# Performance work log

Hardware: AMD Instinct MI355X
Metric: run time of the kernel (lower is better)

Reference implementation:

```python
import jax, jax.numpy as jnp
import numpy as np

N_NODES = 100000
N_EDGES = 1250000
D_IN, D_HID, D_OUT = 64, 32, 41


def setup_inputs() -> dict:
    key = jax.random.key(0)
    ks = jax.random.split(key, 7)
    x = jax.random.normal(ks[0], (N_NODES, D_IN), dtype=jnp.float32)
    edge_index = jax.random.randint(ks[1], (2, N_EDGES), 0, N_NODES, dtype=jnp.int64)
    # PyG SAGEConv params: lin_l (applied to aggregated neighbors, has bias),
    # lin_r (applied to root, no bias). Stored here as [in, out] matrices.
    W1l = jax.random.normal(ks[2], (D_IN, D_HID), dtype=jnp.float32) / np.sqrt(D_IN)
    b1 = jnp.zeros((D_HID,), dtype=jnp.float32)
    W1r = jax.random.normal(ks[3], (D_IN, D_HID), dtype=jnp.float32) / np.sqrt(D_IN)
    W2l = jax.random.normal(ks[4], (D_HID, D_OUT), dtype=jnp.float32) / np.sqrt(D_HID)
    b2 = jnp.zeros((D_OUT,), dtype=jnp.float32)
    W2r = jax.random.normal(ks[5], (D_HID, D_OUT), dtype=jnp.float32) / np.sqrt(D_HID)
    return {"x": x, "edge_index": edge_index, "W1l": W1l, "b1": b1, "W1r": W1r,
            "W2l": W2l, "b2": b2, "W2r": W2r}


def _sage_conv(h, src, dst, n_nodes, Wl, b, Wr):
    # mean-aggregate source features at destination nodes (PyG default aggr='mean')
    msg = h[src]  # [E, d] irregular gather
    agg = jax.ops.segment_sum(msg, dst, num_segments=n_nodes)
    cnt = jax.ops.segment_sum(jnp.ones((src.shape[0],), dtype=h.dtype), dst,
                              num_segments=n_nodes)
    agg = agg / jnp.maximum(cnt, 1.0)[:, None]
    return agg @ Wl + b + h @ Wr


def reference(x, edge_index, W1l, b1, W1r, W2l, b2, W2r):
    src, dst = edge_index[0], edge_index[1]
    n = x.shape[0]
    h = _sage_conv(x, src, dst, n, W1l, b1, W1r)
    h = jax.nn.relu(h)
    # F.dropout(training=self.training) -> identity in eval/inference mode
    out = _sage_conv(h, src, dst, n, W2l, b2, W2r)
    return out
```

## Files before the change

### kernel.cpp

```cpp
#include <hip/hip_runtime.h>

#define N_NODES 100000
#define N_EDGES 1250000
#define D_IN 64
#define D_HID 32
#define D_OUT 41
#define NBUK 784
#define BSH 7
#define BCAP 1920
#define BBLK 192
#define BCHUNK 6511
#define PBLK 1563
#define ROWCAP 48
#define LCAP 52
#define LSTR 88
#define ZERO_OFF 6400000

typedef short bf16x8 __attribute__((ext_vector_type(8)));
typedef float f32x4 __attribute__((ext_vector_type(4)));

__device__ __forceinline__ float bflo(unsigned int u) {
    union { unsigned int i; float f; } v; v.i = u << 16; return v.f;
}
__device__ __forceinline__ float bfhi(unsigned int u) {
    union { unsigned int i; float f; } v; v.i = u & 0xffff0000u; return v.f;
}
__device__ __forceinline__ unsigned short f2bf(float f) {
    union { float f; unsigned int i; } v; v.f = f;
    unsigned int x = v.i;
    return (unsigned short)((x + 0x7fffu + ((x >> 16) & 1u)) >> 16);
}
__device__ __forceinline__ void acc8(float* a, uint4 u) {
    a[0] += bflo(u.x); a[1] += bfhi(u.x);
    a[2] += bflo(u.y); a[3] += bfhi(u.y);
    a[4] += bflo(u.z); a[5] += bfhi(u.z);
    a[6] += bflo(u.w); a[7] += bfhi(u.w);
}

__device__ __forceinline__ void lds_sort(const unsigned int* bk, int total,
                                         int* lists, int* lcnt, int tid) {
    if (tid < 128) lcnt[tid] = 0;
    __syncthreads();
    int i = tid;
    for (; i + 768 < total; i += 1024) {
        unsigned int w0 = bk[i];
        unsigned int w1 = bk[i + 256];
        unsigned int w2 = bk[i + 512];
        unsigned int w3 = bk[i + 768];
        int d0 = (int)(w0 >> 17), s0 = atomicAdd(&lcnt[d0], 1);
        if (s0 < ROWCAP) lists[d0 * LCAP + s0] = (int)((w0 & 0x1FFFFu) << 6);
        int d1 = (int)(w1 >> 17), s1 = atomicAdd(&lcnt[d1], 1);
        if (s1 < ROWCAP) lists[d1 * LCAP + s1] = (int)((w1 & 0x1FFFFu) << 6);
        int d2 = (int)(w2 >> 17), s2 = atomicAdd(&lcnt[d2], 1);
        if (s2 < ROWCAP) lists[d2 * LCAP + s2] = (int)((w2 & 0x1FFFFu) << 6);
        int d3 = (int)(w3 >> 17), s3 = atomicAdd(&lcnt[d3], 1);
        if (s3 < ROWCAP) lists[d3 * LCAP + s3] = (int)((w3 & 0x1FFFFu) << 6);
    }
    for (; i < total; i += 256) {
        unsigned int w = bk[i];
        int dl = (int)(w >> 17);
        int slot = atomicAdd(&lcnt[dl], 1);
        if (slot < ROWCAP) lists[dl * LCAP + slot] = (int)((w & 0x1FFFFu) << 6);
    }
    __syncthreads();
    if (tid < 128) {
        int c = lcnt[tid];
        int cc = c < ROWCAP ? c : ROWCAP;
        int ce = (cc + 15) & ~15; if (ce > ROWCAP) ce = ROWCAP;
        for (int s = cc; s < ce; ++s) lists[tid * LCAP + s] = ZERO_OFF;
    }
    __syncthreads();
}

__device__ __forceinline__ void gather_node(const int* row, int d, const char* tab,
                                            int qb, float* a) {
    int dd = d < ROWCAP ? d : ROWCAP;
    int ddp = (dd + 15) & ~15; if (ddp > ROWCAP) ddp = ROWCAP;
    for (int i = 0; i < ddp; i += 16) {
        int4 o0 = *(const int4*)(row + i);
        int4 o1 = *(const int4*)(row + i + 4);
        int4 o2 = *(const int4*)(row + i + 8);
        int4 o3 = *(const int4*)(row + i + 12);
        uint4 u0 = *(const uint4*)(tab + o0.x + qb);
        uint4 u1 = *(const uint4*)(tab + o0.y + qb);
        uint4 u2 = *(const uint4*)(tab + o0.z + qb);
        uint4 u3 = *(const uint4*)(tab + o0.w + qb);
        uint4 u4 = *(const uint4*)(tab + o1.x + qb);
        uint4 u5 = *(const uint4*)(tab + o1.y + qb);
        uint4 u6 = *(const uint4*)(tab + o1.z + qb);
        uint4 u7 = *(const uint4*)(tab + o1.w + qb);
        uint4 u8 = *(const uint4*)(tab + o2.x + qb);
        uint4 u9 = *(const uint4*)(tab + o2.y + qb);
        uint4 ua = *(const uint4*)(tab + o2.z + qb);
        uint4 ub = *(const uint4*)(tab + o2.w + qb);
        uint4 uc = *(const uint4*)(tab + o3.x + qb);
        uint4 ud = *(const uint4*)(tab + o3.y + qb);
        uint4 ue = *(const uint4*)(tab + o3.z + qb);
        uint4 uf = *(const uint4*)(tab + o3.w + qb);
        acc8(a, u0); acc8(a, u1); acc8(a, u2); acc8(a, u3);
        acc8(a, u4); acc8(a, u5); acc8(a, u6); acc8(a, u7);
        acc8(a, u8); acc8(a, u9); acc8(a, ua); acc8(a, ub);
        acc8(a, uc); acc8(a, ud); acc8(a, ue); acc8(a, uf);
    }
}

__global__ __launch_bounds__(256) void k_front(const int* __restrict__ src,
                                               const int* __restrict__ dst,
                                               unsigned int* __restrict__ bucket_cnt,
                                               unsigned int* __restrict__ buckets,
                                               const float* __restrict__ x,
                                               const float* __restrict__ W1l,
                                               const float* __restrict__ W1r,
                                               const float* __restrict__ b1,
                                               unsigned short* __restrict__ xl,
                                               unsigned short* __restrict__ xr) {
    __shared__ short smem[2 * 64 * LSTR];
    int tid = threadIdx.x;
    if (blockIdx.x < BBLK) {
        int* hist = (int*)smem;
        int* cur  = hist + NBUK;
        for (int i = tid; i < NBUK; i += 256) hist[i] = 0;
        __syncthreads();
        int e0 = blockIdx.x * BCHUNK;
        int e1 = e0 + BCHUNK; if (e1 > N_EDGES) e1 = N_EDGES;
        for (int e = e0 + tid; e < e1; e += 256)
            atomicAdd(&hist[dst[e] >> BSH], 1);
        __syncthreads();
        for (int i = tid; i < NBUK; i += 256)
            cur[i] = (int)atomicAdd(&bucket_cnt[i << 4], (unsigned int)hist[i]);
        __syncthreads();
        for (int e = e0 + tid; e < e1; e += 256) {
            int t = dst[e];
            int b = t >> BSH;
            int pos = atomicAdd(&cur[b], 1);
            if (pos < BCAP)
                buckets[(size_t)b * BCAP + pos] =
                    (unsigned int)src[e] | ((unsigned int)(t & 127) << 17);
        }
        return;
    }
    short* sX  = smem;
    short* sWT = smem + 64 * LSTR;
    int n0 = (blockIdx.x - BBLK) * 64;
    for (int i = tid; i < 64 * 64; i += 256) {
        int col = i >> 6, kk = i & 63;
        float v = (col < 32) ? W1l[kk * 32 + col] : W1r[kk * 32 + (col - 32)];
        sWT[col * LSTR + kk] = (short)f2bf(v);
    }
    {
        int g = tid >> 2, q = tid & 3;
        int n = n0 + g;
        short pk[16];
        if (n < N_NODES) {
            const float4* xr4 = (const float4*)(x + (size_t)n * D_IN + q * 16);
            float4 f0 = xr4[0], f1 = xr4[1], f2 = xr4[2], f3 = xr4[3];
            pk[0] = f2bf(f0.x); pk[1] = f2bf(f0.y); pk[2] = f2bf(f0.z); pk[3] = f2bf(f0.w);
            pk[4] = f2bf(f1.x); pk[5] = f2bf(f1.y); pk[6] = f2bf(f1.z); pk[7] = f2bf(f1.w);
            pk[8] = f2bf(f2.x); pk[9] = f2bf(f2.y); pk[10] = f2bf(f2.z); pk[11] = f2bf(f2.w);
            pk[12] = f2bf(f3.x); pk[13] = f2bf(f3.y); pk[14] = f2bf(f3.z); pk[15] = f2bf(f3.w);
        } else {
            for (int t = 0; t < 16; ++t) pk[t] = 0;
        }
        *(bf16x8*)(sX + g * LSTR + q * 16)     = *(bf16x8*)pk;
        *(bf16x8*)(sX + g * LSTR + q * 16 + 8) = *(bf16x8*)(pk + 8);
    }
    __syncthreads();
    int wid = tid >> 6, lane = tid & 63;
    int quad = lane >> 4, lc = lane & 15;
    int m0 = wid << 4;
    const short* sa = sX + (m0 + lc) * LSTR + quad * 8;
    bf16x8 af0 = *(const bf16x8*)(sa);
    bf16x8 af1 = *(const bf16x8*)(sa + 32);
#pragma unroll
    for (int t = 0; t < 4; ++t) {
        const short* sbp = sWT + (t * 16 + lc) * LSTR + quad * 8;
        bf16x8 bf0 = *(const bf16x8*)(sbp);
        bf16x8 bf1 = *(const bf16x8*)(sbp + 32);
        f32x4 acc = {0.f, 0.f, 0.f, 0.f};
        acc = __builtin_amdgcn_mfma_f32_16x16x32_bf16(af0, bf0, acc, 0, 0, 0);
        acc = __builtin_amdgcn_mfma_f32_16x16x32_bf16(af1, bf1, acc, 0, 0, 0);
        int col = t * 16 + lc;
        float bias = (col >= 32) ? b1[col - 32] : 0.f;
#pragma unroll
        for (int r = 0; r < 4; ++r) {
            int n = n0 + m0 + (quad << 2) + r;
            if (n < N_NODES) {
                if (col < 32) xl[(size_t)n * D_HID + col] = f2bf(acc[r]);
                else          xr[(size_t)n * D_HID + (col - 32)] = f2bf(acc[r] + bias);
            } else if (col < 32) {
                xl[(size_t)n * D_HID + col] = 0;
            }
        }
    }
}

__global__ __launch_bounds__(256) void k_bagg1(const unsigned int* __restrict__ buckets,
                                               const unsigned int* __restrict__ bucket_cnt,
                                               const unsigned short* __restrict__ xl,
                                               const unsigned short* __restrict__ xr,
                                               unsigned short* __restrict__ h) {
    __shared__ int lists[128 * LCAP];
    __shared__ int lcnt[128];
    int tid = threadIdx.x, b = blockIdx.x;
    int total = (int)bucket_cnt[b << 4]; if (total > BCAP) total = BCAP;
    lds_sort(buckets + (size_t)b * BCAP, total, lists, lcnt, tid);
    int nbase = b << BSH;
    int g = tid >> 2, q = tid & 3, qb = q << 4;
    const char* xlb = (const char*)xl;
#pragma unroll
    for (int r0 = 0; r0 < 2; ++r0) {
        int li = g + r0 * 64;
        int n = nbase + li;
        if (n >= N_NODES) {
            if (n < NBUK * 128)
                *(uint4*)((char*)h + ((size_t)n << 6) + qb) = make_uint4(0, 0, 0, 0);
            continue;
        }
        int d = lcnt[li];
        float a[8] = {0.f, 0.f, 0.f, 0.f, 0.f, 0.f, 0.f, 0.f};
        gather_node(lists + li * LCAP, d, xlb, qb, a);
        float inv = 1.0f / fmaxf((float)d, 1.0f);
        uint4 rr = *(const uint4*)((const char*)xr + ((size_t)n << 6) + qb);
        float o0 = fmaxf(a[0] * inv + bflo(rr.x), 0.f);
        float o1 = fmaxf(a[1] * inv + bfhi(rr.x), 0.f);
        float o2 = fmaxf(a[2] * inv + bflo(rr.y), 0.f);
        float o3 = fmaxf(a[3] * inv + bfhi(rr.y), 0.f);
        float o4 = fmaxf(a[4] * inv + bflo(rr.z), 0.f);
        float o5 = fmaxf(a[5] * inv + bfhi(rr.z), 0.f);
        float o6 = fmaxf(a[6] * inv + bflo(rr.w), 0.f);
        float o7 = fmaxf(a[7] * inv + bfhi(rr.w), 0.f);
        uint4 o;
        o.x = ((unsigned int)f2bf(o1) << 16) | f2bf(o0);
        o.y = ((unsigned int)f2bf(o3) << 16) | f2bf(o2);
        o.z = ((unsigned int)f2bf(o5) << 16) | f2bf(o4);
        o.w = ((unsigned int)f2bf(o7) << 16) | f2bf(o6);
        *(uint4*)((char*)h + ((size_t)n << 6) + qb) = o;
    }
}

__global__ __launch_bounds__(256) void k_bagg2(const unsigned int* __restrict__ buckets,
                                               const unsigned int* __restrict__ bucket_cnt,
                                               const unsigned short* __restrict__ h,
                                               const float* __restrict__ W2l,
                                               const float* __restrict__ b2,
                                               const float* __restrict__ W2r,
                                               float* __restrict__ out) {
    __shared__ int lists[128 * LCAP];
    __shared__ int lcnt[128];
    __shared__ short sBT[48 * LSTR];
    __shared__ short sA[64 * LSTR];
    int tid = threadIdx.x, b = blockIdx.x;
    for (int i = tid; i < 48 * 64; i += 256) {
        int col = i >> 6, kk = i & 63;
        float v = 0.f;
        if (col < D_OUT) v = (kk < 32) ? W2l[kk * D_OUT + col] : W2r[(kk - 32) * D_OUT + col];
        sBT[col * LSTR + kk] = (short)f2bf(v);
    }
    int total = (int)bucket_cnt[b << 4]; if (total > BCAP) total = BCAP;
    lds_sort(buckets + (size_t)b * BCAP, total, lists, lcnt, tid);
    int nbase = b << BSH;
    const char* hb = (const char*)h;
    int wid = tid >> 6, lane = tid & 63;
    int quad = lane >> 4, lc = lane & 15;
#pragma unroll
    for (int sub = 0; sub < 2; ++sub) {
        {
            int li = sub * 64 + (tid >> 2);
            int q = tid & 3, qb = q << 4;
            int n = nbase + li;
            bool ok = (n < N_NODES);
            int d = ok ? lcnt[li] : 0;
            float a[8] = {0.f, 0.f, 0.f, 0.f, 0.f, 0.f, 0.f, 0.f};
            if (ok) gather_node(lists + li * LCAP, d, hb, qb, a);
            float inv = 1.0f / fmaxf((float)d, 1.0f);
            short pk[8];
#pragma unroll
            for (int j = 0; j < 8; ++j) pk[j] = (short)f2bf(a[j] * inv);
            uint4 hr = ok ? *(const uint4*)(hb + ((size_t)n << 6) + qb)
                          : make_uint4(0, 0, 0, 0);
            short* sp = sA + (tid >> 2) * LSTR + q * 8;
            *(bf16x8*)(sp)     = *(bf16x8*)pk;
            *(uint4*)(sp + 32) = hr;
        }
        __syncthreads();
        const short* sa = sA + (wid * 16 + lc) * LSTR + quad * 8;
        bf16x8 af0 = *(const bf16x8*)(sa);
        bf16x8 af1 = *(const bf16x8*)(sa + 32);
#pragma unroll
        for (int t = 0; t < 3; ++t) {
            const short* sbp = sBT + (t * 16 + lc) * LSTR + quad * 8;
            bf16x8 bf0 = *(const bf16x8*)(sbp);
            bf16x8 bf1 = *(const bf16x8*)(sbp + 32);
            f32x4 acc = {0.f, 0.f, 0.f, 0.f};
            acc = __builtin_amdgcn_mfma_f32_16x16x32_bf16(af0, bf0, acc, 0, 0, 0);
            acc = __builtin_amdgcn_mfma_f32_16x16x32_bf16(af1, bf1, acc, 0, 0, 0);
            int j = t * 16 + lc;
            if (j < D_OUT) {
                float bias = b2[j];
#pragma unroll
                for (int r = 0; r < 4; ++r) {
                    int n = nbase + sub * 64 + wid * 16 + (quad << 2) + r;
                    if (n < N_NODES) out[(size_t)n * D_OUT + j] = acc[r] + bias;
                }
            }
        }
        __syncthreads();
    }
}

extern "C" void kernel_launch(void* const* d_in, const int* in_sizes, int n_in,
                              void* d_out, int out_size, void* d_ws, size_t ws_size,
                              hipStream_t stream) {
    const float* x   = (const float*)d_in[0];
    const int*   ei  = (const int*)d_in[1];
    const int*   src = ei;
    const int*   dst = ei + N_EDGES;
    const float* W1l = (const float*)d_in[2];
    const float* b1  = (const float*)d_in[3];
    const float* W1r = (const float*)d_in[4];
    const float* W2l = (const float*)d_in[5];
    const float* b2  = (const float*)d_in[6];
    const float* W2r = (const float*)d_in[7];
    float* out = (float*)d_out;

    int* iws = (int*)d_ws;
    unsigned int* bucket_cnt = (unsigned int*)iws;
    unsigned int* buckets = (unsigned int*)(iws + 12544);
    unsigned short* xl = (unsigned short*)(iws + 1517824);
    unsigned short* xr = (unsigned short*)(iws + 3123456);
    unsigned short* h  = (unsigned short*)(iws + 4729088);

    hipMemsetAsync(bucket_cnt, 0, NBUK * 16 * sizeof(int), stream);
    k_front<<<BBLK + PBLK, 256, 0, stream>>>(src, dst, bucket_cnt, buckets,
                                             x, W1l, W1r, b1, xl, xr);
    k_bagg1<<<NBUK, 256, 0, stream>>>(buckets, bucket_cnt, xl, xr, h);
    k_bagg2<<<NBUK, 256, 0, stream>>>(buckets, bucket_cnt, h, W2l, b2, W2r, out);
}
```

Baseline: 185.7 us.

## Reuse sorted adjacency lists across layers, interleave gathers, stage front outputs in LDS

Layer one now writes its per-bucket sorted neighbour lists and counts to global memory, and layer two reads them back instead of re-sorting the buckets in LDS. Both aggregation kernels run the first 16-neighbour chunk for their two nodes back to back, so more independent gathers are in flight. The front projection kernel stages its bf16 outputs in LDS and writes them as coalesced 16-byte rows, and it loads the weights as float4. The cost is extra global traffic for the stored lists, about 24 MB written and read again, and empty rows now always run one padded chunk of loads.

```diff
diff --git a/kernel.cpp b/kernel.cpp
--- a/kernel.cpp
+++ b/kernel.cpp
@@ -14,6 +14,7 @@
 #define ROWCAP 48
 #define LCAP 52
 #define LSTR 88
+#define OSTR 72
 #define ZERO_OFF 6400000
 
 typedef short bf16x8 __attribute__((ext_vector_type(8)));
@@ -66,42 +67,48 @@
     if (tid < 128) {
         int c = lcnt[tid];
         int cc = c < ROWCAP ? c : ROWCAP;
-        int ce = (cc + 15) & ~15; if (ce > ROWCAP) ce = ROWCAP;
+        int ce = (cc + 15) & ~15;
+        if (ce == 0) ce = 16;
+        if (ce > ROWCAP) ce = ROWCAP;
         for (int s = cc; s < ce; ++s) lists[tid * LCAP + s] = ZERO_OFF;
     }
     __syncthreads();
 }
 
-__device__ __forceinline__ void gather_node(const int* row, int d, const char* tab,
-                                            int qb, float* a) {
+__device__ __forceinline__ int padded16(int d) {
     int dd = d < ROWCAP ? d : ROWCAP;
-    int ddp = (dd + 15) & ~15; if (ddp > ROWCAP) ddp = ROWCAP;
-    for (int i = 0; i < ddp; i += 16) {
-        int4 o0 = *(const int4*)(row + i);
-        int4 o1 = *(const int4*)(row + i + 4);
-        int4 o2 = *(const int4*)(row + i + 8);
-        int4 o3 = *(const int4*)(row + i + 12);
-        uint4 u0 = *(const uint4*)(tab + o0.x + qb);
-        uint4 u1 = *(const uint4*)(tab + o0.y + qb);
-        uint4 u2 = *(const uint4*)(tab + o0.z + qb);
-        uint4 u3 = *(const uint4*)(tab + o0.w + qb);
-        uint4 u4 = *(const uint4*)(tab + o1.x + qb);
-        uint4 u5 = *(const uint4*)(tab + o1.y + qb);
-        uint4 u6 = *(const uint4*)(tab + o1.z + qb);
-        uint4 u7 = *(const uint4*)(tab + o1.w + qb);
-        uint4 u8 = *(const uint4*)(tab + o2.x + qb);
-        uint4 u9 = *(const uint4*)(tab + o2.y + qb);
-        uint4 ua = *(const uint4*)(tab + o2.z + qb);
-        uint4 ub = *(const uint4*)(tab + o2.w + qb);
-        uint4 uc = *(const uint4*)(tab + o3.x + qb);
-        uint4 ud = *(const uint4*)(tab + o3.y + qb);
-        uint4 ue = *(const uint4*)(tab + o3.z + qb);
-        uint4 uf = *(const uint4*)(tab + o3.w + qb);
-        acc8(a, u0); acc8(a, u1); acc8(a, u2); acc8(a, u3);
-        acc8(a, u4); acc8(a, u5); acc8(a, u6); acc8(a, u7);
-        acc8(a, u8); acc8(a, u9); acc8(a, ua); acc8(a, ub);
-        acc8(a, uc); acc8(a, ud); acc8(a, ue); acc8(a, uf);
-    }
+    int ddp = (dd + 15) & ~15;
+    if (ddp == 0) ddp = 16;
+    if (ddp > ROWCAP) ddp = ROWCAP;
+    return ddp;
+}
+
+__device__ __forceinline__ void chunk16(const int* row, int i, const char* tab,
+                                        int qb, float* a) {
+    int4 o0 = *(const int4*)(row + i);
+    int4 o1 = *(const int4*)(row + i + 4);
+    int4 o2 = *(const int4*)(row + i + 8);
+    int4 o3 = *(const int4*)(row + i + 12);
+    uint4 u0 = *(const uint4*)(tab + o0.x + qb);
+    uint4 u1 = *(const uint4*)(tab + o0.y + qb);
+    uint4 u2 = *(const uint4*)(tab + o0.z + qb);
+    uint4 u3 = *(const uint4*)(tab + o0.w + qb);
+    uint4 u4 = *(const uint4*)(tab + o1.x + qb);
+    uint4 u5 = *(const uint4*)(tab + o1.y + qb);
+    uint4 u6 = *(const uint4*)(tab + o1.z + qb);
+    uint4 u7 = *(const uint4*)(tab + o1.w + qb);
+    uint4 u8 = *(const uint4*)(tab + o2.x + qb);
+    uint4 u9 = *(const uint4*)(tab + o2.y + qb);
+    uint4 ua = *(const uint4*)(tab + o2.z + qb);
+    uint4 ub = *(const uint4*)(tab + o2.w + qb);
+    uint4 uc = *(const uint4*)(tab + o3.x + qb);
+    uint4 ud = *(const uint4*)(tab + o3.y + qb);
+    uint4 ue = *(const uint4*)(tab + o3.z + qb);
+    uint4 uf = *(const uint4*)(tab + o3.w + qb);
+    acc8(a, u0); acc8(a, u1); acc8(a, u2); acc8(a, u3);
+    acc8(a, u4); acc8(a, u5); acc8(a, u6); acc8(a, u7);
+    acc8(a, u8); acc8(a, u9); acc8(a, ua); acc8(a, ub);
+    acc8(a, uc); acc8(a, ud); acc8(a, ue); acc8(a, uf);
 }
 
 __global__ __launch_bounds__(256) void k_front(const int* __restrict__ src,
@@ -142,10 +149,15 @@
     short* sX  = smem;
     short* sWT = smem + 64 * LSTR;
     int n0 = (blockIdx.x - BBLK) * 64;
-    for (int i = tid; i < 64 * 64; i += 256) {
-        int col = i >> 6, kk = i & 63;
-        float v = (col < 32) ? W1l[kk * 32 + col] : W1r[kk * 32 + (col - 32)];
-        sWT[col * LSTR + kk] = (short)f2bf(v);
+    for (int i = tid; i < 1024; i += 256) {
+        int k = i >> 4, c4 = i & 15;
+        float4 v = (c4 < 8) ? ((const float4*)W1l)[k * 8 + c4]
+                            : ((const float4*)W1r)[k * 8 + (c4 - 8)];
+        int col = c4 * 4;
+        sWT[(col + 0) * LSTR + k] = (short)f2bf(v.x);
+        sWT[(col + 1) * LSTR + k] = (short)f2bf(v.y);
+        sWT[(col + 2) * LSTR + k] = (short)f2bf(v.z);
+        sWT[(col + 3) * LSTR + k] = (short)f2bf(v.w);
     }
     {
         int g = tid >> 2, q = tid & 3;
@@ -171,6 +183,8 @@
     const short* sa = sX + (m0 + lc) * LSTR + quad * 8;
     bf16x8 af0 = *(const bf16x8*)(sa);
     bf16x8 af1 = *(const bf16x8*)(sa + 32);
+    __syncthreads();
+    short* sO = sX;
 #pragma unroll
     for (int t = 0; t < 4; ++t) {
         const short* sbp = sWT + (t * 16 + lc) * LSTR + quad * 8;
@@ -182,15 +196,23 @@
         int col = t * 16 + lc;
         float bias = (col >= 32) ? b1[col - 32] : 0.f;
 #pragma unroll
-        for (int r = 0; r < 4; ++r) {
-            int n = n0 + m0 + (quad << 2) + r;
-            if (n < N_NODES) {
-                if (col < 32) xl[(size_t)n * D_HID + col] = f2bf(acc[r]);
-                else          xr[(size_t)n * D_HID + (col - 32)] = f2bf(acc[r] + bias);
-            } else if (col < 32) {
-                xl[(size_t)n * D_HID + col] = 0;
-            }
-        }
+        for (int r = 0; r < 4; ++r)
+            sO[(m0 + (quad << 2) + r) * OSTR + col] = (short)f2bf(acc[r] + bias);
+    }
+    __syncthreads();
+    {
+        int g = tid >> 2, q = tid & 3;
+        int n = n0 + g;
+        uint4 vl, vr;
+        if (n < N_NODES) {
+            vl = *(const uint4*)(sO + g * OSTR + q * 8);
+            vr = *(const uint4*)(sO + g * OSTR + 32 + q * 8);
+        } else {
+            vl = make_uint4(0, 0, 0, 0);
+            vr = make_uint4(0, 0, 0, 0);
+        }
+        *(uint4*)((char*)xl + ((size_t)n << 6) + (q << 4)) = vl;
+        *(uint4*)((char*)xr + ((size_t)n << 6) + (q << 4)) = vr;
     }
 }
 
@@ -198,37 +220,54 @@
                                                const unsigned int* __restrict__ bucket_cnt,
                                                const unsigned short* __restrict__ xl,
                                                const unsigned short* __restrict__ xr,
-                                               unsigned short* __restrict__ h) {
+                                               unsigned short* __restrict__ h,
+                                               int* __restrict__ glists,
+                                               int* __restrict__ gcnt) {
     __shared__ int lists[128 * LCAP];
     __shared__ int lcnt[128];
     int tid = threadIdx.x, b = blockIdx.x;
     int total = (int)bucket_cnt[b << 4]; if (total > BCAP) total = BCAP;
     lds_sort(buckets + (size_t)b * BCAP, total, lists, lcnt, tid);
     int nbase = b << BSH;
+    for (int i4 = tid; i4 < 128 * 12; i4 += 256) {
+        int li = i4 / 12, c4 = i4 % 12;
+        uint4 v = *(const uint4*)(lists + li * LCAP + c4 * 4);
+        *(uint4*)(glists + (size_t)(nbase + li) * ROWCAP + c4 * 4) = v;
+    }
+    if (tid < 128) gcnt[nbase + tid] = lcnt[tid];
     int g = tid >> 2, q = tid & 3, qb = q << 4;
+    int liA = g, liB = g + 64;
+    int nA = nbase + liA, nB = nbase + liB;
+    int dA = lcnt[liA], dB = lcnt[liB];
+    int pA = padded16(dA), pB = padded16(dB);
+    const int* rowA = lists + liA * LCAP;
+    const int* rowB = lists + liB * LCAP;
     const char* xlb = (const char*)xl;
-#pragma unroll
-    for (int r0 = 0; r0 < 2; ++r0) {
-        int li = g + r0 * 64;
-        int n = nbase + li;
+    float a[8] = {0.f, 0.f, 0.f, 0.f, 0.f, 0.f, 0.f, 0.f};
+    float c[8] = {0.f, 0.f, 0.f, 0.f, 0.f, 0.f, 0.f, 0.f};
+    chunk16(rowA, 0, xlb, qb, a);
+    chunk16(rowB, 0, xlb, qb, c);
+    for (int i = 16; i < pA; i += 16) chunk16(rowA, i, xlb, qb, a);
+    for (int i = 16; i < pB; i += 16) chunk16(rowB, i, xlb, qb, c);
+#pragma unroll
+    for (int half = 0; half < 2; ++half) {
+        int n = half ? nB : nA;
+        int d = half ? dB : dA;
+        const float* ar = half ? c : a;
         if (n >= N_NODES) {
-            if (n < NBUK * 128)
-                *(uint4*)((char*)h + ((size_t)n << 6) + qb) = make_uint4(0, 0, 0, 0);
+            *(uint4*)((char*)h + ((size_t)n << 6) + qb) = make_uint4(0, 0, 0, 0);
             continue;
         }
-        int d = lcnt[li];
-        float a[8] = {0.f, 0.f, 0.f, 0.f, 0.f, 0.f, 0.f, 0.f};
-        gather_node(lists + li * LCAP, d, xlb, qb, a);
         float inv = 1.0f / fmaxf((float)d, 1.0f);
         uint4 rr = *(const uint4*)((const char*)xr + ((size_t)n << 6) + qb);
-        float o0 = fmaxf(a[0] * inv + bflo(rr.x), 0.f);
-        float o1 = fmaxf(a[1] * inv + bfhi(rr.x), 0.f);
-        float o2 = fmaxf(a[2] * inv + bflo(rr.y), 0.f);
-        float o3 = fmaxf(a[3] * inv + bfhi(rr.y), 0.f);
-        float o4 = fmaxf(a[4] * inv + bflo(rr.z), 0.f);
-        float o5 = fmaxf(a[5] * inv + bfhi(rr.z), 0.f);
-        float o6 = fmaxf(a[6] * inv + bflo(rr.w), 0.f);
-        float o7 = fmaxf(a[7] * inv + bfhi(rr.w), 0.f);
+        float o0 = fmaxf(ar[0] * inv + bflo(rr.x), 0.f);
+        float o1 = fmaxf(ar[1] * inv + bfhi(rr.x), 0.f);
+        float o2 = fmaxf(ar[2] * inv + bflo(rr.y), 0.f);
+        float o3 = fmaxf(ar[3] * inv + bfhi(rr.y), 0.f);
+        float o4 = fmaxf(ar[4] * inv + bflo(rr.z), 0.f);
+        float o5 = fmaxf(ar[5] * inv + bfhi(rr.z), 0.f);
+        float o6 = fmaxf(ar[6] * inv + bflo(rr.w), 0.f);
+        float o7 = fmaxf(ar[7] * inv + bfhi(rr.w), 0.f);
         uint4 o;
         o.x = ((unsigned int)f2bf(o1) << 16) | f2bf(o0);
         o.y = ((unsigned int)f2bf(o3) << 16) | f2bf(o2);
@@ -238,8 +277,8 @@
     }
 }
 
-__global__ __launch_bounds__(256) void k_bagg2(const unsigned int* __restrict__ buckets,
-                                               const unsigned int* __restrict__ bucket_cnt,
+__global__ __launch_bounds__(256) void k_bagg2(const int* __restrict__ glists,
+                                               const int* __restrict__ gcnt,
                                                const unsigned short* __restrict__ h,
                                                const float* __restrict__ W2l,
                                                const float* __restrict__ b2,
@@ -250,35 +289,49 @@
     __shared__ short sBT[48 * LSTR];
     __shared__ short sA[64 * LSTR];
     int tid = threadIdx.x, b = blockIdx.x;
+    int nbase = b << BSH;
     for (int i = tid; i < 48 * 64; i += 256) {
         int col = i >> 6, kk = i & 63;
         float v = 0.f;
         if (col < D_OUT) v = (kk < 32) ? W2l[kk * D_OUT + col] : W2r[(kk - 32) * D_OUT + col];
         sBT[col * LSTR + kk] = (short)f2bf(v);
     }
-    int total = (int)bucket_cnt[b << 4]; if (total > BCAP) total = BCAP;
-    lds_sort(buckets + (size_t)b * BCAP, total, lists, lcnt, tid);
-    int nbase = b << BSH;
+    for (int i4 = tid; i4 < 128 * 12; i4 += 256) {
+        int li = i4 / 12, c4 = i4 % 12;
+        uint4 v = *(const uint4*)(glists + (size_t)(nbase + li) * ROWCAP + c4 * 4);
+        *(uint4*)(lists + li * LCAP + c4 * 4) = v;
+    }
+    if (tid < 128) lcnt[tid] = gcnt[nbase + tid];
+    __syncthreads();
+    int g = tid >> 2, q = tid & 3, qb = q << 4;
+    int liA = g, liB = g + 64;
+    int dA = lcnt[liA], dB = lcnt[liB];
+    int pA = padded16(dA), pB = padded16(dB);
+    const int* rowA = lists + liA * LCAP;
+    const int* rowB = lists + liB * LCAP;
     const char* hb = (const char*)h;
+    float a[8] = {0.f, 0.f, 0.f, 0.f, 0.f, 0.f, 0.f, 0.f};
+    float c[8] = {0.f, 0.f, 0.f, 0.f, 0.f, 0.f, 0.f, 0.f};
+    chunk16(rowA, 0, hb, qb, a);
+    chunk16(rowB, 0, hb, qb, c);
+    for (int i = 16; i < pA; i += 16) chunk16(rowA, i, hb, qb, a);
+    for (int i = 16; i < pB; i += 16) chunk16(rowB, i, hb, qb, c);
     int wid = tid >> 6, lane = tid & 63;
     int quad = lane >> 4, lc = lane & 15;
 #pragma unroll
     for (int sub = 0; sub < 2; ++sub) {
         {
-            int li = sub * 64 + (tid >> 2);
-            int q = tid & 3, qb = q << 4;
-            int n = nbase + li;
+            int n = nbase + sub * 64 + g;
             bool ok = (n < N_NODES);
-            int d = ok ? lcnt[li] : 0;
-            float a[8] = {0.f, 0.f, 0.f, 0.f, 0.f, 0.f, 0.f, 0.f};
-            if (ok) gather_node(lists + li * LCAP, d, hb, qb, a);
+            int d = sub ? dB : dA;
+            const float* ar = sub ? c : a;
             float inv = 1.0f / fmaxf((float)d, 1.0f);
             short pk[8];
 #pragma unroll
-            for (int j = 0; j < 8; ++j) pk[j] = (short)f2bf(a[j] * inv);
+            for (int j = 0; j < 8; ++j) pk[j] = (short)f2bf(ar[j] * inv);
             uint4 hr = ok ? *(const uint4*)(hb + ((size_t)n << 6) + qb)
                           : make_uint4(0, 0, 0, 0);
-            short* sp = sA + (tid >> 2) * LSTR + q * 8;
+            short* sp = sA + g * LSTR + q * 8;
             *(bf16x8*)(sp)     = *(bf16x8*)pk;
             *(uint4*)(sp + 32) = hr;
         }
@@ -326,13 +379,16 @@
     int* iws = (int*)d_ws;
     unsigned int* bucket_cnt = (unsigned int*)iws;
     unsigned int* buckets = (unsigned int*)(iws + 12544);
-    unsigned short* xl = (unsigned short*)(iws + 1517824);
-    unsigned short* xr = (unsigned short*)(iws + 3123456);
-    unsigned short* h  = (unsigned short*)(iws + 4729088);
+    int* gcnt   = iws + 1517824;
+    int* glists = iws + 1618176;
+    unsigned short* xl = (unsigned short*)(iws + 6435072);
+    unsigned short* xr = (unsigned short*)(iws + 8040704);
+    unsigned short* h  = (unsigned short*)(iws + 9646336);
 
     hipMemsetAsync(bucket_cnt, 0, NBUK * 16 * sizeof(int), stream);
     k_front<<<BBLK + PBLK, 256, 0, stream>>>(src, dst, bucket_cnt, buckets,
                                              x, W1l, W1r, b1, xl, xr);
-    k_bagg1<<<NBUK, 256, 0, stream>>>(buckets, bucket_cnt, xl, xr, h);
-    k_bagg2<<<NBUK, 256, 0, stream>>>(buckets, bucket_cnt, h, W2l, b2, W2r, out);
-}
+    k_bagg1<<<NBUK, 256, 0, stream>>>(buckets, bucket_cnt, xl, xr, h,
+                                      glists, gcnt);
+    k_bagg2<<<NBUK, 256, 0, stream>>>(glists, gcnt, h, W2l, b2, W2r, out);
+}
```

After: 185.4 us. Within noise of the previous version (-0.2%).
